# Kernel tuning notes

Hardware: AMD Instinct MI355X
Metric: run time of the kernel (lower is better)

## Reference

```python
import jax, jax.numpy as jnp
import numpy as np

N_NODES = 100000
N_EDGES = 1600000
IN_CH = 165
HID = 128


def _xavier(key, shape):
    fan_out, fan_in = shape
    lim = float(np.sqrt(6.0 / (fan_in + fan_out)))
    return jax.random.uniform(key, shape, jnp.float32, -lim, lim)


def setup_inputs() -> dict:
    key = jax.random.key(0)
    ks = jax.random.split(key, 8)
    x = jax.random.normal(ks[0], (N_NODES, IN_CH), jnp.float32)
    edge_index = jax.random.randint(ks[1], (2, N_EDGES), 0, N_NODES, jnp.int64)
    return {
        "x": x,
        "edge_index": edge_index,
        "W_l0": _xavier(ks[2], (HID, IN_CH)),
        "b_l0": jnp.zeros((HID,), jnp.float32),
        "W_r0": _xavier(ks[3], (HID, IN_CH)),
        "W_l1": _xavier(ks[4], (HID, HID)),
        "b_l1": jnp.zeros((HID,), jnp.float32),
        "W_r1": _xavier(ks[5], (HID, HID)),
        "W_l2": _xavier(ks[6], (HID, HID)),
        "b_l2": jnp.zeros((HID,), jnp.float32),
        "W_r2": _xavier(ks[7], (HID, HID)),
        "W_out": _xavier(jax.random.fold_in(key, 7), (2, HID)),
        "b_out": jnp.zeros((2,), jnp.float32),
    }


def _sage_conv(x, src, dst, W_l, b_l, W_r):
    # mean-aggregate source features into destination nodes
    msg = x[src]  # [E, d] gather
    agg = jax.ops.segment_sum(msg, dst, num_segments=N_NODES)  # [N, d]
    cnt = jax.ops.segment_sum(jnp.ones((src.shape[0], 1), x.dtype), dst,
                              num_segments=N_NODES)
    mean = agg / jnp.maximum(cnt, 1.0)
    # out = lin_l(mean) + lin_r(x); lin_r has no bias (PyG SAGEConv)
    return mean @ W_l.T + b_l + x @ W_r.T


def reference(x, edge_index, W_l0, b_l0, W_r0, W_l1, b_l1, W_r1,
              W_l2, b_l2, W_r2, W_out, b_out):
    src, dst = edge_index[0], edge_index[1]
    h = jax.nn.relu(_sage_conv(x, src, dst, W_l0, b_l0, W_r0))
    h = jax.nn.relu(_sage_conv(h, src, dst, W_l1, b_l1, W_r1))
    h = _sage_conv(h, src, dst, W_l2, b_l2, W_r2)
    # dropout is identity in inference
    return h @ W_out.T + b_out  # [N, 2]
```

## Files before the change

### kernel.cpp

```cpp
#include <hip/hip_runtime.h>
#include <cstdint>
#include <cstddef>

#define NN 100000
#define IN_CH 165
#define HID 128

#define NBUCK 196
#define NPB 512
#define BMAX 10240
#define NWG 256

typedef __attribute__((ext_vector_type(8))) short short8;
typedef __attribute__((ext_vector_type(4))) float f32x4;

__device__ __forceinline__ ushort f2bf(float v) {
    uint b = __builtin_bit_cast(uint, v);
    return (ushort)((b + 0x7FFFu + ((b >> 16) & 1u)) >> 16);
}
__device__ __forceinline__ float bf2f(ushort u) {
    uint b = ((uint)u) << 16;
    return __builtin_bit_cast(float, b);
}
__device__ __forceinline__ float lo16f(uint u) { return __builtin_bit_cast(float, u << 16); }
__device__ __forceinline__ float hi16f(uint u) { return __builtin_bit_cast(float, u & 0xFFFF0000u); }

__global__ __launch_bounds__(256) void k_cnt(const int* __restrict__ dst, int E, int chunk,
                                             int* __restrict__ cnt) {
    __shared__ int h[NBUCK];
    const int w = blockIdx.x, t = threadIdx.x;
    for (int b = t; b < NBUCK; b += 256) h[b] = 0;
    __syncthreads();
    const int beg = w * chunk, end = min(E, beg + chunk);
    for (int i = beg + t; i < end; i += 256) atomicAdd(&h[dst[i] >> 9], 1);
    __syncthreads();
    for (int b = t; b < NBUCK; b += 256) cnt[w * NBUCK + b] = h[b];
}

__global__ __launch_bounds__(1024) void k_cscan(const int* __restrict__ cnt,
                                                int* __restrict__ gaddr) {
    __shared__ int ps[1024];
    const int t = threadIdx.x;
    int s = 0;
    for (int k = 0; k < 49; k++) {
        const int m = t * 49 + k;
        s += cnt[(m & (NWG - 1)) * NBUCK + (m >> 8)];
    }
    ps[t] = s;
    __syncthreads();
    for (int off = 1; off < 1024; off <<= 1) {
        int v = (t >= off) ? ps[t - off] : 0;
        __syncthreads();
        ps[t] += v;
        __syncthreads();
    }
    int run = (t > 0) ? ps[t - 1] : 0;
    for (int k = 0; k < 49; k++) {
        const int m = t * 49 + k;
        gaddr[m] = run;
        run += cnt[(m & (NWG - 1)) * NBUCK + (m >> 8)];
    }
}

__global__ __launch_bounds__(256) void k_scatter(const int* __restrict__ src,
                                                 const int* __restrict__ dst, int E, int chunk,
                                                 const int* __restrict__ gaddr,
                                                 int* __restrict__ bdata) {
    __shared__ int cur[NBUCK];
    __shared__ int thist[256];
    __shared__ int sA[256];
    __shared__ int tex[NBUCK];
    __shared__ int lpos[NBUCK];
    __shared__ int staged[2048];
    __shared__ int addrs[2048];
    const int w = blockIdx.x, t = threadIdx.x;
    for (int b = t; b < NBUCK; b += 256) cur[b] = gaddr[b * NWG + w];
    const int beg = w * chunk, end = min(E, beg + chunk);
    for (int tb = beg; tb < end; tb += 2048) {
        const int tcnt = min(2048, end - tb);
        int key[8], bk[8];
#pragma unroll
        for (int j = 0; j < 8; j++) {
            const int i = tb + j * 256 + t;
            if (i < end) {
                const int d = dst[i];
                bk[j] = d >> 9;
                key[j] = (src[i] << 9) | (d & 511);
            } else bk[j] = -1;
        }
        __syncthreads();
        thist[t] = 0;
        __syncthreads();
#pragma unroll
        for (int j = 0; j < 8; j++)
            if (bk[j] >= 0) atomicAdd(&thist[bk[j]], 1);
        __syncthreads();
        sA[t] = thist[t];
        __syncthreads();
        for (int off = 1; off < 256; off <<= 1) {
            int v = (t >= off) ? sA[t - off] : 0;
            __syncthreads();
            sA[t] += v;
            __syncthreads();
        }
        if (t < NBUCK) {
            const int e = sA[t] - thist[t];
            tex[t] = e;
            lpos[t] = e;
        }
        __syncthreads();
#pragma unroll
        for (int j = 0; j < 8; j++)
            if (bk[j] >= 0) {
                const int b = bk[j];
                const int l = atomicAdd(&lpos[b], 1);
                staged[l] = key[j];
                addrs[l] = cur[b] + (l - tex[b]);
            }
        __syncthreads();
        for (int l = t; l < tcnt; l += 256) bdata[addrs[l]] = staged[l];
        __syncthreads();
        if (t < NBUCK) cur[t] += thist[t];
    }
}

__global__ __launch_bounds__(256) void k_csr2(const int* __restrict__ gaddr,
                                              const int* __restrict__ bdata, int E,
                                              int* __restrict__ csr, int* __restrict__ row_off,
                                              float* __restrict__ inv, int N) {
    __shared__ int keys[BMAX];
    __shared__ int sorted[BMAX];
    __shared__ int h5[NPB];
    __shared__ int s5[NPB];
    const int b = blockIdx.x, t = threadIdx.x;
    const int base = gaddr[b * NWG];
    const int nxt = (b == NBUCK - 1) ? E : gaddr[(b + 1) * NWG];
    const int tot = min(nxt - base, BMAX);
    for (int i = t; i < tot; i += 256) keys[i] = bdata[base + i];
    h5[t] = 0;
    h5[t + 256] = 0;
    __syncthreads();
    for (int i = t; i < tot; i += 256) atomicAdd(&h5[keys[i] & 511], 1);
    __syncthreads();
    s5[t] = h5[t];
    s5[t + 256] = h5[t + 256];
    __syncthreads();
    for (int off = 1; off < 512; off <<= 1) {
        const int a = (t >= off) ? s5[t - off] : 0;
        const int c = (t + 256 >= off) ? s5[t + 256 - off] : 0;
        __syncthreads();
        s5[t] += a;
        s5[t + 256] += c;
        __syncthreads();
    }
    const int e0 = s5[t] - h5[t];
    const int e1 = s5[t + 256] - h5[t + 256];
    __syncthreads();
    s5[t] = e0;
    s5[t + 256] = e1;
    const int n0 = b * NPB + t, n1 = b * NPB + t + 256;
    if (n0 < N) { row_off[n0] = base + e0; inv[n0] = 1.0f / (float)max(h5[t], 1); }
    if (n1 < N) { row_off[n1] = base + e1; inv[n1] = 1.0f / (float)max(h5[t + 256], 1); }
    if (b == 0 && t == 0) row_off[N] = E;
    __syncthreads();
    for (int i = t; i < tot; i += 256) {
        const int k = keys[i];
        const int p = atomicAdd(&s5[k & 511], 1);
        sorted[p] = k;
    }
    __syncthreads();
    for (int i = t; i < tot; i += 256) csr[base + i] = sorted[i] >> 9;
}

__device__ __forceinline__ void wpack_one(const float* __restrict__ W, int K, int idx,
                                          ushort* __restrict__ Wh) {
    const int k = idx >> 7;
    const int j = idx & 127;
    const float v = (k < K) ? W[j * K + k] : 0.0f;
    const int o = (k >> 3) * (HID * 8) + j * 8 + (k & 7);
    Wh[o] = f2bf(v);
}

__global__ __launch_bounds__(256) void k_prep(
    const float* __restrict__ Wl0, const float* __restrict__ Wr0,
    const float* __restrict__ Wl1, const float* __restrict__ Wr1,
    const float* __restrict__ Wl2, const float* __restrict__ Wr2,
    const float* __restrict__ Wout, const float* __restrict__ bl2,
    const float* __restrict__ bout,
    ushort* __restrict__ Wl0h, ushort* __restrict__ Wr0h,
    ushort* __restrict__ Wl1h, ushort* __restrict__ Wr1h,
    float* __restrict__ Wzp, float* __restrict__ bz)
{
    if (blockIdx.x == 96) {
        const int t = threadIdx.x;
        const int c = t >> 7, k = t & 127;
        float sl = 0.f, sr = 0.f;
        for (int j = 0; j < 128; j++) {
            const float wo = Wout[c * 128 + j];
            sl += wo * Wl2[j * 128 + k];
            sr += wo * Wr2[j * 128 + k];
        }
        Wzp[c * 128 + k] = sl;
        Wzp[256 + c * 128 + k] = sr;
        if (t < 2) {
            float s = bout[t];
            for (int j = 0; j < 128; j++) s += Wout[t * 128 + j] * bl2[j];
            bz[t] = s;
        }
        return;
    }
    const int gid = blockIdx.x * 256 + threadIdx.x;
    if (gid < 192 * HID) {
        wpack_one(Wl0, IN_CH, gid, Wl0h);
        wpack_one(Wr0, IN_CH, gid, Wr0h);
    }
    if (gid < 128 * HID) {
        wpack_one(Wl1, HID, gid, Wl1h);
        wpack_one(Wr1, HID, gid, Wr1h);
    }
}

template <typename TIN, int K, int KP>
__global__ __launch_bounds__(256) void k_gemm_mfma(
    const TIN* __restrict__ h,
    const ushort* __restrict__ Wlh, const ushort* __restrict__ Wrh,
    ushort* __restrict__ yl, ushort* __restrict__ yr)
{
    constexpr int RS = KP * 2;
    __shared__ __align__(16) char Ah[32 * RS];
    const int tid = threadIdx.x;
    const int node0 = blockIdx.x * 32;
    const TIN* __restrict__ hp = h + (size_t)node0 * K;

    if constexpr (sizeof(TIN) == 2) {
        constexpr int Q = 32 * (KP / 8);
        for (int q = tid; q < Q; q += 256) {
            const int r = q / (KP / 8);
            const int kp = (q - r * (KP / 8)) * 8;
            const short8 v = *reinterpret_cast<const short8*>(&hp[r * K + kp]);
            const int byte = r * RS + ((kp * 2) ^ ((r & 7) << 4));
            *reinterpret_cast<short8*>(Ah + byte) = v;
        }
    } else {
        constexpr int Q = 32 * (KP / 4);
        for (int q = tid; q < Q; q += 256) {
            const int r = q / (KP / 4);
            const int kp = (q - r * (KP / 4)) * 4;
            float v0, v1, v2, v3;
            if constexpr (K % 4 == 0) {
                const float4 v = *reinterpret_cast<const float4*>(&hp[r * K + kp]);
                v0 = v.x; v1 = v.y; v2 = v.z; v3 = v.w;
            } else {
                v0 = (kp + 0 < K) ? hp[r * K + kp + 0] : 0.0f;
                v1 = (kp + 1 < K) ? hp[r * K + kp + 1] : 0.0f;
                v2 = (kp + 2 < K) ? hp[r * K + kp + 2] : 0.0f;
                v3 = (kp + 3 < K) ? hp[r * K + kp + 3] : 0.0f;
            }
            const int byte = r * RS + ((kp * 2) ^ ((r & 7) << 4));
            *reinterpret_cast<ushort4*>(Ah + byte) =
                make_ushort4(f2bf(v0), f2bf(v1), f2bf(v2), f2bf(v3));
        }
    }
    __syncthreads();

    const int lane = tid & 63;
    const int w = tid >> 6;
    const int trow = lane & 15;
    const int kg = lane >> 4;
    const ushort* __restrict__ Bh = (w & 1) ? Wrh : Wlh;
    ushort* __restrict__ yo = (w & 1) ? yr : yl;
    const int cb0 = (w >> 1) * 4;

    f32x4 acc[2][4];
#pragma unroll
    for (int a = 0; a < 2; ++a)
#pragma unroll
        for (int b = 0; b < 4; ++b) acc[a][b] = (f32x4){0.f, 0.f, 0.f, 0.f};

    const int xo = (trow & 7) << 4;
    const char* __restrict__ pA0 = Ah + trow * RS;
    const char* __restrict__ pA1 = Ah + (trow + 16) * RS;

    constexpr int KS = KP / 32;
    for (int ks = 0; ks < KS; ++ks) {
        const int kbyte = (ks * 64 + kg * 16) ^ xo;
        const short8 a0h = *reinterpret_cast<const short8*>(pA0 + kbyte);
        const short8 a1h = *reinterpret_cast<const short8*>(pA1 + kbyte);
        const int bbase = (ks * 4 + kg) * (HID * 8) + trow * 8;
#pragma unroll
        for (int ci = 0; ci < 4; ++ci) {
            const short8 bh = *reinterpret_cast<const short8*>(Bh + bbase + (cb0 + ci) * 128);
            acc[0][ci] = __builtin_amdgcn_mfma_f32_16x16x32_bf16(a0h, bh, acc[0][ci], 0, 0, 0);
            acc[1][ci] = __builtin_amdgcn_mfma_f32_16x16x32_bf16(a1h, bh, acc[1][ci], 0, 0, 0);
        }
    }

#pragma unroll
    for (int rb = 0; rb < 2; ++rb) {
        const int nb_ = node0 + rb * 16 + kg * 4;
#pragma unroll
        for (int ci = 0; ci < 4; ++ci) {
            const int col = (cb0 + ci) * 16 + trow;
            const f32x4 a = acc[rb][ci];
#pragma unroll
            for (int rr = 0; rr < 4; ++rr)
                yo[(size_t)(nb_ + rr) * HID + col] = f2bf(a[rr]);
        }
    }
}

template <int HEAD>
__global__ __launch_bounds__(256) void k_agg2(
    const ushort* __restrict__ yl, const int* __restrict__ row_off,
    const int* __restrict__ csr, const float* __restrict__ inv,
    const float* __restrict__ bias, const ushort* __restrict__ yr,
    ushort* __restrict__ hout, const float* __restrict__ Wzp,
    float2* __restrict__ zb, float2* __restrict__ rb, int N)
{
    const int wid = (blockIdx.x * 256 + (int)threadIdx.x) >> 6;
    const int lane = threadIdx.x & 63;
    if (wid >= N) return;
    const int eslot = lane >> 4;
    const int c = lane & 15;
    const int beg = row_off[wid];
    const int end = row_off[wid + 1];
    const uint4* __restrict__ Y = (const uint4*)yl;

    float a0 = 0.f, a1 = 0.f, a2 = 0.f, a3 = 0.f;
    float a4 = 0.f, a5 = 0.f, a6 = 0.f, a7 = 0.f;
    auto acc8 = [&](uint4 u) {
        a0 += lo16f(u.x); a1 += hi16f(u.x);
        a2 += lo16f(u.y); a3 += hi16f(u.y);
        a4 += lo16f(u.z); a5 += hi16f(u.z);
        a6 += lo16f(u.w); a7 += hi16f(u.w);
    };

    int e = beg;
    for (; e + 16 <= end; e += 16) {
        const int s0 = csr[e + eslot];
        const int s1 = csr[e + 4 + eslot];
        const int s2 = csr[e + 8 + eslot];
        const int s3 = csr[e + 12 + eslot];
        const uint4 u0 = Y[(size_t)s0 * 16 + c];
        const uint4 u1 = Y[(size_t)s1 * 16 + c];
        const uint4 u2 = Y[(size_t)s2 * 16 + c];
        const uint4 u3 = Y[(size_t)s3 * 16 + c];
        acc8(u0); acc8(u1); acc8(u2); acc8(u3);
    }
    if (e + 8 <= end) {
        const int s0 = csr[e + eslot];
        const int s1 = csr[e + 4 + eslot];
        const uint4 u0 = Y[(size_t)s0 * 16 + c];
        const uint4 u1 = Y[(size_t)s1 * 16 + c];
        acc8(u0); acc8(u1);
        e += 8;
    }
    if (e + 4 <= end) {
        const uint4 u0 = Y[(size_t)csr[e + eslot] * 16 + c];
        acc8(u0);
        e += 4;
    }
    if (e + eslot < end) {
        const uint4 u0 = Y[(size_t)csr[e + eslot] * 16 + c];
        acc8(u0);
    }

    a0 += __shfl_xor(a0, 16); a1 += __shfl_xor(a1, 16);
    a2 += __shfl_xor(a2, 16); a3 += __shfl_xor(a3, 16);
    a4 += __shfl_xor(a4, 16); a5 += __shfl_xor(a5, 16);
    a6 += __shfl_xor(a6, 16); a7 += __shfl_xor(a7, 16);
    a0 += __shfl_xor(a0, 32); a1 += __shfl_xor(a1, 32);
    a2 += __shfl_xor(a2, 32); a3 += __shfl_xor(a3, 32);
    a4 += __shfl_xor(a4, 32); a5 += __shfl_xor(a5, 32);
    a6 += __shfl_xor(a6, 32); a7 += __shfl_xor(a7, 32);

    if (lane < 16) {
        const float iv = inv[wid];
        const uint4 rv = ((const uint4*)yr)[(size_t)wid * 16 + lane];
        const float4 b0 = ((const float4*)bias)[lane * 2];
        const float4 b1 = ((const float4*)bias)[lane * 2 + 1];
        const float v0 = fmaxf(a0 * iv + b0.x + lo16f(rv.x), 0.f);
        const float v1 = fmaxf(a1 * iv + b0.y + hi16f(rv.x), 0.f);
        const float v2 = fmaxf(a2 * iv + b0.z + lo16f(rv.y), 0.f);
        const float v3 = fmaxf(a3 * iv + b0.w + hi16f(rv.y), 0.f);
        const float v4 = fmaxf(a4 * iv + b1.x + lo16f(rv.z), 0.f);
        const float v5 = fmaxf(a5 * iv + b1.y + hi16f(rv.z), 0.f);
        const float v6 = fmaxf(a6 * iv + b1.z + lo16f(rv.w), 0.f);
        const float v7 = fmaxf(a7 * iv + b1.w + hi16f(rv.w), 0.f);
        if constexpr (!HEAD) {
            uint4 o;
            o.x = (uint)f2bf(v0) | ((uint)f2bf(v1) << 16);
            o.y = (uint)f2bf(v2) | ((uint)f2bf(v3) << 16);
            o.z = (uint)f2bf(v4) | ((uint)f2bf(v5) << 16);
            o.w = (uint)f2bf(v6) | ((uint)f2bf(v7) << 16);
            ((uint4*)hout)[(size_t)wid * 16 + lane] = o;
        } else {
            const int ch = lane * 8;
            float z0 = 0.f, z1 = 0.f, r0 = 0.f, r1 = 0.f;
            const float vv[8] = {v0, v1, v2, v3, v4, v5, v6, v7};
#pragma unroll
            for (int j = 0; j < 8; j++) {
                z0 += vv[j] * Wzp[ch + j];
                z1 += vv[j] * Wzp[128 + ch + j];
                r0 += vv[j] * Wzp[256 + ch + j];
                r1 += vv[j] * Wzp[384 + ch + j];
            }
#pragma unroll
            for (int off = 8; off > 0; off >>= 1) {
                z0 += __shfl_xor(z0, off);
                z1 += __shfl_xor(z1, off);
                r0 += __shfl_xor(r0, off);
                r1 += __shfl_xor(r1, off);
            }
            if (lane == 0) {
                zb[wid] = make_float2(z0, z1);
                rb[wid] = make_float2(r0, r1);
            }
        }
    }
}

__global__ __launch_bounds__(256) void k_aggz(
    const float2* __restrict__ z, const float2* __restrict__ r,
    const int* __restrict__ row_off, const int* __restrict__ csr,
    const float* __restrict__ inv, const float* __restrict__ bz,
    float2* __restrict__ out, int N)
{
    const int node = (blockIdx.x * 256 + (int)threadIdx.x) >> 6;
    const int lane = threadIdx.x & 63;
    if (node >= N) return;
    const int beg = row_off[node];
    const int end = row_off[node + 1];
    float s0 = 0.f, s1 = 0.f;
    for (int e = beg + lane; e < end; e += 64) {
        const float2 v = z[csr[e]];
        s0 += v.x;
        s1 += v.y;
    }
#pragma unroll
    for (int off = 32; off > 0; off >>= 1) {
        s0 += __shfl_xor(s0, off);
        s1 += __shfl_xor(s1, off);
    }
    if (lane == 0) {
        const float iv = inv[node];
        const float2 rv = r[node];
        out[node] = make_float2(s0 * iv + rv.x + bz[0], s1 * iv + rv.y + bz[1]);
    }
}

extern "C" void kernel_launch(void* const* d_in, const int* in_sizes, int n_in,
                              void* d_out, int out_size, void* d_ws, size_t ws_size,
                              hipStream_t stream) {
    const float* x    = (const float*)d_in[0];
    const int*   ei   = (const int*)d_in[1];
    const float* Wl0  = (const float*)d_in[2];
    const float* bl0  = (const float*)d_in[3];
    const float* Wr0  = (const float*)d_in[4];
    const float* Wl1  = (const float*)d_in[5];
    const float* bl1  = (const float*)d_in[6];
    const float* Wr1  = (const float*)d_in[7];
    const float* Wl2  = (const float*)d_in[8];
    const float* bl2  = (const float*)d_in[9];
    const float* Wr2  = (const float*)d_in[10];
    const float* Wout = (const float*)d_in[11];
    const float* bout = (const float*)d_in[12];

    const int N = NN;
    const int E = in_sizes[1] / 2;
    const int* src = ei;
    const int* dst = ei + E;
    const int chunk = (E + NWG - 1) / NWG;

    char* w = (char*)d_ws;
    auto alloc = [&](size_t bytes) {
        char* p = w;
        w += (bytes + 255) & ~(size_t)255;
        return p;
    };
    int*    cnt     = (int*)alloc((size_t)NWG * NBUCK * 4);
    int*    gaddr   = (int*)alloc((size_t)NWG * NBUCK * 4);
    int*    bdata   = (int*)alloc((size_t)E * 4);
    int*    row_off = (int*)alloc((size_t)(N + 1) * 4);
    float*  inv     = (float*)alloc((size_t)N * 4);
    int*    csr     = (int*)alloc((size_t)E * 4);
    ushort* Wl0h    = (ushort*)alloc((size_t)192 * HID * 2);
    ushort* Wr0h    = (ushort*)alloc((size_t)192 * HID * 2);
    ushort* Wl1h    = (ushort*)alloc((size_t)HID * HID * 2);
    ushort* Wr1h    = (ushort*)alloc((size_t)HID * HID * 2);
    float*  Wzp     = (float*)alloc((size_t)512 * 4);
    float*  bz      = (float*)alloc((size_t)8 * 4);
    ushort* B0      = (ushort*)alloc((size_t)N * HID * 2);
    ushort* B1      = (ushort*)alloc((size_t)N * HID * 2);
    ushort* B2      = (ushort*)alloc((size_t)N * HID * 2);
    float*  zbuf    = (float*)alloc((size_t)N * 2 * 4);
    float*  rbuf    = (float*)alloc((size_t)N * 2 * 4);

    k_cnt<<<NWG, 256, 0, stream>>>(dst, E, chunk, cnt);
    k_cscan<<<1, 1024, 0, stream>>>(cnt, gaddr);
    k_scatter<<<NWG, 256, 0, stream>>>(src, dst, E, chunk, gaddr, bdata);
    k_csr2<<<NBUCK, 256, 0, stream>>>(gaddr, bdata, E, csr, row_off, inv, N);

    k_prep<<<97, 256, 0, stream>>>(Wl0, Wr0, Wl1, Wr1, Wl2, Wr2, Wout, bl2, bout,
                                   Wl0h, Wr0h, Wl1h, Wr1h, Wzp, bz);

    const int gemm_grid = N / 32;
    const int wave_grid = N / 4;

    k_gemm_mfma<float, IN_CH, 192><<<gemm_grid, 256, 0, stream>>>(x, Wl0h, Wr0h, B0, B1);
    k_agg2<0><<<wave_grid, 256, 0, stream>>>(B0, row_off, csr, inv, bl0, B1, B1,
                                             nullptr, nullptr, nullptr, N);

    k_gemm_mfma<ushort, HID, HID><<<gemm_grid, 256, 0, stream>>>(B1, Wl1h, Wr1h, B0, B2);
    k_agg2<1><<<wave_grid, 256, 0, stream>>>(B0, row_off, csr, inv, bl1, B2, nullptr,
                                             Wzp, (float2*)zbuf, (float2*)rbuf, N);

    k_aggz<<<wave_grid, 256, 0, stream>>>((const float2*)zbuf, (const float2*)rbuf,
                                          row_off, csr, inv, bz, (float2*)d_out, N);
}
```

Baseline: 322.7 us.

## Vectorize edge loads, transpose count layout, stage fp32 GEMM input, cache head weights

The edge-count and scatter kernels now read dst/src with int4 vector loads over 8 contiguous edges per thread, and the chunk size is rounded to a multiple of 8 so the loads stay aligned. The per-workgroup count table is stored bucket-major, which makes the scan read it contiguously. The fp32 layer-0 GEMM first copies its raw 32x165 tile into LDS with float4 loads before converting to bf16, replacing scalar unaligned global reads. The templated aggregation kernel is split into a ReLU variant and a head variant, and the head variant caches its projection weights in shared memory. The costs are more LDS use in the GEMM plus an extra barrier, and changed edge order inside each bucket.

```diff
diff --git a/kernel.cpp b/kernel.cpp
--- a/kernel.cpp
+++ b/kernel.cpp
@@ -17,10 +17,6 @@
 __device__ __forceinline__ ushort f2bf(float v) {
     uint b = __builtin_bit_cast(uint, v);
     return (ushort)((b + 0x7FFFu + ((b >> 16) & 1u)) >> 16);
-}
-__device__ __forceinline__ float bf2f(ushort u) {
-    uint b = ((uint)u) << 16;
-    return __builtin_bit_cast(float, b);
 }
 __device__ __forceinline__ float lo16f(uint u) { return __builtin_bit_cast(float, u << 16); }
 __device__ __forceinline__ float hi16f(uint u) { return __builtin_bit_cast(float, u & 0xFFFF0000u); }
@@ -32,9 +28,24 @@
     for (int b = t; b < NBUCK; b += 256) h[b] = 0;
     __syncthreads();
     const int beg = w * chunk, end = min(E, beg + chunk);
-    for (int i = beg + t; i < end; i += 256) atomicAdd(&h[dst[i] >> 9], 1);
-    __syncthreads();
-    for (int b = t; b < NBUCK; b += 256) cnt[w * NBUCK + b] = h[b];
+    for (int i0 = beg + t * 8; i0 < end; i0 += 2048) {
+        if (i0 + 8 <= end) {
+            const int4 d0 = *reinterpret_cast<const int4*>(dst + i0);
+            const int4 d1 = *reinterpret_cast<const int4*>(dst + i0 + 4);
+            atomicAdd(&h[d0.x >> 9], 1);
+            atomicAdd(&h[d0.y >> 9], 1);
+            atomicAdd(&h[d0.z >> 9], 1);
+            atomicAdd(&h[d0.w >> 9], 1);
+            atomicAdd(&h[d1.x >> 9], 1);
+            atomicAdd(&h[d1.y >> 9], 1);
+            atomicAdd(&h[d1.z >> 9], 1);
+            atomicAdd(&h[d1.w >> 9], 1);
+        } else {
+            for (int i = i0; i < end; ++i) atomicAdd(&h[dst[i] >> 9], 1);
+        }
+    }
+    __syncthreads();
+    for (int b = t; b < NBUCK; b += 256) cnt[b * NWG + w] = h[b];
 }
 
 __global__ __launch_bounds__(1024) void k_cscan(const int* __restrict__ cnt,
@@ -42,10 +53,7 @@
     __shared__ int ps[1024];
     const int t = threadIdx.x;
     int s = 0;
-    for (int k = 0; k < 49; k++) {
-        const int m = t * 49 + k;
-        s += cnt[(m & (NWG - 1)) * NBUCK + (m >> 8)];
-    }
+    for (int k = 0; k < 49; k++) s += cnt[t * 49 + k];
     ps[t] = s;
     __syncthreads();
     for (int off = 1; off < 1024; off <<= 1) {
@@ -58,7 +66,7 @@
     for (int k = 0; k < 49; k++) {
         const int m = t * 49 + k;
         gaddr[m] = run;
-        run += cnt[(m & (NWG - 1)) * NBUCK + (m >> 8)];
+        run += cnt[m];
     }
 }
 
@@ -79,14 +87,30 @@
     for (int tb = beg; tb < end; tb += 2048) {
         const int tcnt = min(2048, end - tb);
         int key[8], bk[8];
-#pragma unroll
-        for (int j = 0; j < 8; j++) {
-            const int i = tb + j * 256 + t;
-            if (i < end) {
-                const int d = dst[i];
-                bk[j] = d >> 9;
-                key[j] = (src[i] << 9) | (d & 511);
-            } else bk[j] = -1;
+        const int i0 = tb + t * 8;
+        if (i0 + 8 <= end) {
+            const int4 d0 = *reinterpret_cast<const int4*>(dst + i0);
+            const int4 d1 = *reinterpret_cast<const int4*>(dst + i0 + 4);
+            const int4 s0 = *reinterpret_cast<const int4*>(src + i0);
+            const int4 s1 = *reinterpret_cast<const int4*>(src + i0 + 4);
+            bk[0] = d0.x >> 9; key[0] = (s0.x << 9) | (d0.x & 511);
+            bk[1] = d0.y >> 9; key[1] = (s0.y << 9) | (d0.y & 511);
+            bk[2] = d0.z >> 9; key[2] = (s0.z << 9) | (d0.z & 511);
+            bk[3] = d0.w >> 9; key[3] = (s0.w << 9) | (d0.w & 511);
+            bk[4] = d1.x >> 9; key[4] = (s1.x << 9) | (d1.x & 511);
+            bk[5] = d1.y >> 9; key[5] = (s1.y << 9) | (d1.y & 511);
+            bk[6] = d1.z >> 9; key[6] = (s1.z << 9) | (d1.z & 511);
+            bk[7] = d1.w >> 9; key[7] = (s1.w << 9) | (d1.w & 511);
+        } else {
+#pragma unroll
+            for (int j = 0; j < 8; j++) {
+                const int i = i0 + j;
+                if (i < end) {
+                    const int d = dst[i];
+                    bk[j] = d >> 9;
+                    key[j] = (src[i] << 9) | (d & 511);
+                } else bk[j] = -1;
+            }
         }
         __syncthreads();
         thist[t] = 0;
@@ -242,20 +266,19 @@
             *reinterpret_cast<short8*>(Ah + byte) = v;
         }
     } else {
-        constexpr int Q = 32 * (KP / 4);
-        for (int q = tid; q < Q; q += 256) {
-            const int r = q / (KP / 4);
-            const int kp = (q - r * (KP / 4)) * 4;
-            float v0, v1, v2, v3;
-            if constexpr (K % 4 == 0) {
-                const float4 v = *reinterpret_cast<const float4*>(&hp[r * K + kp]);
-                v0 = v.x; v1 = v.y; v2 = v.z; v3 = v.w;
-            } else {
-                v0 = (kp + 0 < K) ? hp[r * K + kp + 0] : 0.0f;
-                v1 = (kp + 1 < K) ? hp[r * K + kp + 1] : 0.0f;
-                v2 = (kp + 2 < K) ? hp[r * K + kp + 2] : 0.0f;
-                v3 = (kp + 3 < K) ? hp[r * K + kp + 3] : 0.0f;
-            }
+        __shared__ __align__(16) float raw[32 * K];
+        const float* __restrict__ hpf = (const float*)hp;
+        for (int i = tid * 4; i < 32 * K; i += 1024)
+            *reinterpret_cast<float4*>(&raw[i]) = *reinterpret_cast<const float4*>(&hpf[i]);
+        __syncthreads();
+        constexpr int G = KP / 4;
+        for (int q = tid; q < 32 * G; q += 256) {
+            const int r = q / G;
+            const int kp = (q - r * G) * 4;
+            const float v0 = (kp + 0 < K) ? raw[r * K + kp + 0] : 0.0f;
+            const float v1 = (kp + 1 < K) ? raw[r * K + kp + 1] : 0.0f;
+            const float v2 = (kp + 2 < K) ? raw[r * K + kp + 2] : 0.0f;
+            const float v3 = (kp + 3 < K) ? raw[r * K + kp + 3] : 0.0f;
             const int byte = r * RS + ((kp * 2) ^ ((r & 7) << 4));
             *reinterpret_cast<ushort4*>(Ah + byte) =
                 make_ushort4(f2bf(v0), f2bf(v1), f2bf(v2), f2bf(v3));
@@ -309,13 +332,12 @@
     }
 }
 
-template <int HEAD>
-__global__ __launch_bounds__(256) void k_agg2(
+
+__global__ __launch_bounds__(256) void k_agg_relu(
     const ushort* __restrict__ yl, const int* __restrict__ row_off,
     const int* __restrict__ csr, const float* __restrict__ inv,
     const float* __restrict__ bias, const ushort* __restrict__ yr,
-    ushort* __restrict__ hout, const float* __restrict__ Wzp,
-    float2* __restrict__ zb, float2* __restrict__ rb, int N)
+    ushort* __restrict__ hout, int N)
 {
     const int wid = (blockIdx.x * 256 + (int)threadIdx.x) >> 6;
     const int lane = threadIdx.x & 63;
@@ -387,35 +409,116 @@
         const float v5 = fmaxf(a5 * iv + b1.y + hi16f(rv.z), 0.f);
         const float v6 = fmaxf(a6 * iv + b1.z + lo16f(rv.w), 0.f);
         const float v7 = fmaxf(a7 * iv + b1.w + hi16f(rv.w), 0.f);
-        if constexpr (!HEAD) {
-            uint4 o;
-            o.x = (uint)f2bf(v0) | ((uint)f2bf(v1) << 16);
-            o.y = (uint)f2bf(v2) | ((uint)f2bf(v3) << 16);
-            o.z = (uint)f2bf(v4) | ((uint)f2bf(v5) << 16);
-            o.w = (uint)f2bf(v6) | ((uint)f2bf(v7) << 16);
-            ((uint4*)hout)[(size_t)wid * 16 + lane] = o;
-        } else {
-            const int ch = lane * 8;
-            float z0 = 0.f, z1 = 0.f, r0 = 0.f, r1 = 0.f;
-            const float vv[8] = {v0, v1, v2, v3, v4, v5, v6, v7};
-#pragma unroll
-            for (int j = 0; j < 8; j++) {
-                z0 += vv[j] * Wzp[ch + j];
-                z1 += vv[j] * Wzp[128 + ch + j];
-                r0 += vv[j] * Wzp[256 + ch + j];
-                r1 += vv[j] * Wzp[384 + ch + j];
-            }
-#pragma unroll
-            for (int off = 8; off > 0; off >>= 1) {
-                z0 += __shfl_xor(z0, off);
-                z1 += __shfl_xor(z1, off);
-                r0 += __shfl_xor(r0, off);
-                r1 += __shfl_xor(r1, off);
-            }
-            if (lane == 0) {
-                zb[wid] = make_float2(z0, z1);
-                rb[wid] = make_float2(r0, r1);
-            }
+        uint4 o;
+        o.x = (uint)f2bf(v0) | ((uint)f2bf(v1) << 16);
+        o.y = (uint)f2bf(v2) | ((uint)f2bf(v3) << 16);
+        o.z = (uint)f2bf(v4) | ((uint)f2bf(v5) << 16);
+        o.w = (uint)f2bf(v6) | ((uint)f2bf(v7) << 16);
+        ((uint4*)hout)[(size_t)wid * 16 + lane] = o;
+    }
+}
+
+__global__ __launch_bounds__(256) void k_agg_head(
+    const ushort* __restrict__ yl, const int* __restrict__ row_off,
+    const int* __restrict__ csr, const float* __restrict__ inv,
+    const float* __restrict__ bias, const ushort* __restrict__ yr,
+    const float* __restrict__ Wzp, float2* __restrict__ zb,
+    float2* __restrict__ rb, int N)
+{
+    __shared__ float wz[512];
+    for (int i = threadIdx.x; i < 512; i += 256) wz[i] = Wzp[i];
+    __syncthreads();
+
+    const int wid = (blockIdx.x * 256 + (int)threadIdx.x) >> 6;
+    const int lane = threadIdx.x & 63;
+    if (wid >= N) return;
+    const int eslot = lane >> 4;
+    const int c = lane & 15;
+    const int beg = row_off[wid];
+    const int end = row_off[wid + 1];
+    const uint4* __restrict__ Y = (const uint4*)yl;
+
+    float a0 = 0.f, a1 = 0.f, a2 = 0.f, a3 = 0.f;
+    float a4 = 0.f, a5 = 0.f, a6 = 0.f, a7 = 0.f;
+    auto acc8 = [&](uint4 u) {
+        a0 += lo16f(u.x); a1 += hi16f(u.x);
+        a2 += lo16f(u.y); a3 += hi16f(u.y);
+        a4 += lo16f(u.z); a5 += hi16f(u.z);
+        a6 += lo16f(u.w); a7 += hi16f(u.w);
+    };
+
+    int e = beg;
+    for (; e + 16 <= end; e += 16) {
+        const int s0 = csr[e + eslot];
+        const int s1 = csr[e + 4 + eslot];
+        const int s2 = csr[e + 8 + eslot];
+        const int s3 = csr[e + 12 + eslot];
+        const uint4 u0 = Y[(size_t)s0 * 16 + c];
+        const uint4 u1 = Y[(size_t)s1 * 16 + c];
+        const uint4 u2 = Y[(size_t)s2 * 16 + c];
+        const uint4 u3 = Y[(size_t)s3 * 16 + c];
+        acc8(u0); acc8(u1); acc8(u2); acc8(u3);
+    }
+    if (e + 8 <= end) {
+        const int s0 = csr[e + eslot];
+        const int s1 = csr[e + 4 + eslot];
+        const uint4 u0 = Y[(size_t)s0 * 16 + c];
+        const uint4 u1 = Y[(size_t)s1 * 16 + c];
+        acc8(u0); acc8(u1);
+        e += 8;
+    }
+    if (e + 4 <= end) {
+        const uint4 u0 = Y[(size_t)csr[e + eslot] * 16 + c];
+        acc8(u0);
+        e += 4;
+    }
+    if (e + eslot < end) {
+        const uint4 u0 = Y[(size_t)csr[e + eslot] * 16 + c];
+        acc8(u0);
+    }
+
+    a0 += __shfl_xor(a0, 16); a1 += __shfl_xor(a1, 16);
+    a2 += __shfl_xor(a2, 16); a3 += __shfl_xor(a3, 16);
+    a4 += __shfl_xor(a4, 16); a5 += __shfl_xor(a5, 16);
+    a6 += __shfl_xor(a6, 16); a7 += __shfl_xor(a7, 16);
+    a0 += __shfl_xor(a0, 32); a1 += __shfl_xor(a1, 32);
+    a2 += __shfl_xor(a2, 32); a3 += __shfl_xor(a3, 32);
+    a4 += __shfl_xor(a4, 32); a5 += __shfl_xor(a5, 32);
+    a6 += __shfl_xor(a6, 32); a7 += __shfl_xor(a7, 32);
+
+    if (lane < 16) {
+        const float iv = inv[wid];
+        const uint4 rv = ((const uint4*)yr)[(size_t)wid * 16 + lane];
+        const float4 b0 = ((const float4*)bias)[lane * 2];
+        const float4 b1 = ((const float4*)bias)[lane * 2 + 1];
+        const float v0 = fmaxf(a0 * iv + b0.x + lo16f(rv.x), 0.f);
+        const float v1 = fmaxf(a1 * iv + b0.y + hi16f(rv.x), 0.f);
+        const float v2 = fmaxf(a2 * iv + b0.z + lo16f(rv.y), 0.f);
+        const float v3 = fmaxf(a3 * iv + b0.w + hi16f(rv.y), 0.f);
+        const float v4 = fmaxf(a4 * iv + b1.x + lo16f(rv.z), 0.f);
+        const float v5 = fmaxf(a5 * iv + b1.y + hi16f(rv.z), 0.f);
+        const float v6 = fmaxf(a6 * iv + b1.z + lo16f(rv.w), 0.f);
+        const float v7 = fmaxf(a7 * iv + b1.w + hi16f(rv.w), 0.f);
+        const int ch = lane * 8;
+        float z0 = 0.f, z1 = 0.f, r0 = 0.f, r1 = 0.f;
+        const float vv[8] = {v0, v1, v2, v3, v4, v5, v6, v7};
+#pragma unroll
+        for (int j = 0; j < 8; j++) {
+            z0 += vv[j] * wz[ch + j];
+            z1 += vv[j] * wz[128 + ch + j];
+            r0 += vv[j] * wz[256 + ch + j];
+            r1 += vv[j] * wz[384 + ch + j];
+        }
+#pragma unroll
+        for (int off = 8; off > 0; off >>= 1) {
+            z0 += __shfl_xor(z0, off);
+            z1 += __shfl_xor(z1, off);
+            r0 += __shfl_xor(r0, off);
+            r1 += __shfl_xor(r1, off);
+        }
+        if (lane == 0) {
+            zb[wid] = make_float2(z0, z1);
+            rb[wid] = make_float2(r0, r1);
         }
     }
 }
@@ -470,7 +573,7 @@
     const int E = in_sizes[1] / 2;
     const int* src = ei;
     const int* dst = ei + E;
-    const int chunk = (E + NWG - 1) / NWG;
+    const int chunk = (((E + NWG - 1) / NWG) + 7) & ~7;
 
     char* w = (char*)d_ws;
     auto alloc = [&](size_t bytes) {
@@ -508,12 +611,11 @@
     const int wave_grid = N / 4;
 
     k_gemm_mfma<float, IN_CH, 192><<<gemm_grid, 256, 0, stream>>>(x, Wl0h, Wr0h, B0, B1);
-    k_agg2<0><<<wave_grid, 256, 0, stream>>>(B0, row_off, csr, inv, bl0, B1, B1,
-                                             nullptr, nullptr, nullptr, N);
+    k_agg_relu<<<wave_grid, 256, 0, stream>>>(B0, row_off, csr, inv, bl0, B1, B1, N);
 
     k_gemm_mfma<ushort, HID, HID><<<gemm_grid, 256, 0, stream>>>(B1, Wl1h, Wr1h, B0, B2);
-    k_agg2<1><<<wave_grid, 256, 0, stream>>>(B0, row_off, csr, inv, bl1, B2, nullptr,
-                                             Wzp, (float2*)zbuf, (float2*)rbuf, N);
+    k_agg_head<<<wave_grid, 256, 0, stream>>>(B0, row_off, csr, inv, bl1, B2,
+                                              Wzp, (float2*)zbuf, (float2*)rbuf, N);
 
     k_aggz<<<wave_grid, 256, 0, stream>>>((const float2*)zbuf, (const float2*)rbuf,
                                           row_off, csr, inv, bz, (float2*)d_out, N);
```

Result: faster. 285.4 us (-11.5%).
